# Optimization experiments

Hardware: AMD Instinct MI355X
Metric: run time of the kernel (lower is better)

The kernel has to match this reference:

```python
import jax, jax.numpy as jnp
import numpy as np

B, C, L = 4, 64, 4096

def setup_inputs() -> dict:
    key = jax.random.key(0)
    ks = jax.random.split(key, 7)
    s = 1.0 / np.sqrt(C)
    return {
        "x": jax.random.normal(ks[0], (B, C, L), dtype=jnp.float32),
        "wq": jax.random.uniform(ks[1], (C, C), jnp.float32, -s, s),
        "bq": jax.random.uniform(ks[2], (C,), jnp.float32, -s, s),
        "wk": jax.random.uniform(ks[3], (C, C), jnp.float32, -s, s),
        "bk": jax.random.uniform(ks[4], (C,), jnp.float32, -s, s),
        "wv": jax.random.uniform(ks[5], (C, C), jnp.float32, -s, s),
        "bv": jax.random.uniform(ks[6], (C,), jnp.float32, -s, s),
    }

def reference(x, wq, bq, wk, bk, wv, bv):
    # x: [B, C, L]; conv1d kernel-size-1 == per-position linear over channels.
    scale = jnp.sqrt(jnp.asarray(x.shape[1], x.dtype))
    # project and move to [B, L, C]
    q = jnp.einsum('oc,bcl->blo', wq, x) + bq  # [B, L, C]
    k = jnp.einsum('oc,bcl->blo', wk, x) + bk
    v = jnp.einsum('oc,bcl->blo', wv, x) + bv
    attn = jnp.einsum('bic,bjc->bij', q, k) / scale  # [B, L, L]
    attn = jax.nn.softmax(attn, axis=-1)
    out = jnp.einsum('bij,bjc->bic', attn, v)  # [B, L, C]
    return out.transpose(0, 2, 1) + x  # back to [B, C, L] with residual
```

## Files before the change

### kernel.cpp

```cpp
#include <hip/hip_runtime.h>
#include <hip/hip_bf16.h>

typedef float    f32x4  __attribute__((ext_vector_type(4)));
typedef float    f32x16 __attribute__((ext_vector_type(16)));
typedef short    s16x4  __attribute__((ext_vector_type(4)));
typedef short    s16x8  __attribute__((ext_vector_type(8)));
typedef unsigned u32x4  __attribute__((ext_vector_type(4)));
typedef __bf16   bf16x8 __attribute__((ext_vector_type(8)));

#define DEVI __device__ __forceinline__

DEVI short f2bf(float f) {
    unsigned u = __builtin_bit_cast(unsigned, f);
    u += 0x8000u;
    return (short)(u >> 16);
}
DEVI float bf2f(short s) {
    return __builtin_bit_cast(float, ((unsigned)(unsigned short)s) << 16);
}
DEVI unsigned cvt_pk_bf16(float lo, float hi) {
#if defined(__HIP_DEVICE_COMPILE__)
    unsigned r;
    asm("v_cvt_pk_bf16_f32 %0, %1, %2" : "=v"(r) : "v"(lo), "v"(hi));
    return r;
#else
    return (unsigned)(unsigned short)f2bf(lo) | ((unsigned)(unsigned short)f2bf(hi) << 16);
#endif
}

DEVI float fast_exp2(float x) {
#if defined(__HIP_DEVICE_COMPILE__) && __has_builtin(__builtin_amdgcn_exp2f)
    return __builtin_amdgcn_exp2f(x);
#else
    return exp2f(x);
#endif
}

DEVI f32x4 mfma32(s16x8 a, s16x8 b, f32x4 c) {
#if defined(__HIP_DEVICE_COMPILE__) && __has_builtin(__builtin_amdgcn_mfma_f32_16x16x32_bf16)
    return __builtin_amdgcn_mfma_f32_16x16x32_bf16(
        __builtin_bit_cast(bf16x8, a), __builtin_bit_cast(bf16x8, b), c, 0, 0, 0);
#else
    asm volatile("v_mfma_f32_16x16x32_bf16 %0, %1, %2, %0" : "+v"(c) : "v"(a), "v"(b));
    return c;
#endif
}

DEVI f32x16 mfma3216(s16x8 a, s16x8 b, f32x16 c) {
#if defined(__HIP_DEVICE_COMPILE__) && __has_builtin(__builtin_amdgcn_mfma_f32_32x32x16_bf16)
    return __builtin_amdgcn_mfma_f32_32x32x16_bf16(
        __builtin_bit_cast(bf16x8, a), __builtin_bit_cast(bf16x8, b), c, 0, 0, 0);
#else
    asm volatile("v_mfma_f32_32x32x16_bf16 %0, %1, %2, %0" : "+v"(c) : "v"(a), "v"(b));
    return c;
#endif
}

DEVI void setprio1() {
#if defined(__HIP_DEVICE_COMPILE__)
    __builtin_amdgcn_s_setprio(1);
#endif
}
DEVI void setprio0() {
#if defined(__HIP_DEVICE_COMPILE__)
    __builtin_amdgcn_s_setprio(0);
#endif
}

__global__ __launch_bounds__(512) void qkv_proj(
    const float* __restrict__ x,
    const float* __restrict__ wq, const float* __restrict__ bq,
    const float* __restrict__ wk, const float* __restrict__ bk,
    const float* __restrict__ wv, const float* __restrict__ bv,
    short* __restrict__ Qg, short* __restrict__ Kg, short* __restrict__ Vtg)
{
    __shared__ short Xt[32 * 64];

    const int b  = blockIdx.x >> 7;
    const int l0 = (blockIdx.x & 127) * 32;
    const int t  = threadIdx.x;
    const float QS = 0.18033688011112042f;

    {
        const int c  = t & 63;
        const int lh = (t >> 6) * 4;
        const float* xr = x + ((size_t)b * 64 + c) * 4096 + l0 + lh;
        const float4 x0 = *reinterpret_cast<const float4*>(xr);
        float xv[4] = {x0.x, x0.y, x0.z, x0.w};
        #pragma unroll
        for (int i = 0; i < 4; ++i) {
            const int l = lh + i;
            Xt[l * 64 + (((c >> 3) ^ (l & 7)) * 8) + (c & 7)] = f2bf(xv[i]);
        }
    }

    const int lane = t & 63, w = t >> 6;
    const int g = lane >> 4, col = lane & 15;
    const int o0 = (w & 3) * 16;
    const int h  = w >> 2;

    s16x8 wqf[2], wkf[2], wvf[2];
    #pragma unroll
    for (int kc = 0; kc < 2; ++kc) {
        const int cb = 8 * g + 32 * kc;
        const float4 q0 = *reinterpret_cast<const float4*>(wq + (o0 + col) * 64 + cb);
        const float4 q1 = *reinterpret_cast<const float4*>(wq + (o0 + col) * 64 + cb + 4);
        const float4 k0 = *reinterpret_cast<const float4*>(wk + (o0 + col) * 64 + cb);
        const float4 k1 = *reinterpret_cast<const float4*>(wk + (o0 + col) * 64 + cb + 4);
        const float4 v0 = *reinterpret_cast<const float4*>(wv + (o0 + col) * 64 + cb);
        const float4 v1 = *reinterpret_cast<const float4*>(wv + (o0 + col) * 64 + cb + 4);
        wqf[kc][0] = f2bf(q0.x * QS); wqf[kc][1] = f2bf(q0.y * QS);
        wqf[kc][2] = f2bf(q0.z * QS); wqf[kc][3] = f2bf(q0.w * QS);
        wqf[kc][4] = f2bf(q1.x * QS); wqf[kc][5] = f2bf(q1.y * QS);
        wqf[kc][6] = f2bf(q1.z * QS); wqf[kc][7] = f2bf(q1.w * QS);
        wkf[kc][0] = f2bf(k0.x); wkf[kc][1] = f2bf(k0.y);
        wkf[kc][2] = f2bf(k0.z); wkf[kc][3] = f2bf(k0.w);
        wkf[kc][4] = f2bf(k1.x); wkf[kc][5] = f2bf(k1.y);
        wkf[kc][6] = f2bf(k1.z); wkf[kc][7] = f2bf(k1.w);
        wvf[kc][0] = f2bf(v0.x); wvf[kc][1] = f2bf(v0.y);
        wvf[kc][2] = f2bf(v0.z); wvf[kc][3] = f2bf(v0.w);
        wvf[kc][4] = f2bf(v1.x); wvf[kc][5] = f2bf(v1.y);
        wvf[kc][6] = f2bf(v1.z); wvf[kc][7] = f2bf(v1.w);
    }
    const f32x4 bq4 = *reinterpret_cast<const f32x4*>(bq + o0 + 4 * g);
    const f32x4 bk4 = *reinterpret_cast<const f32x4*>(bk + o0 + 4 * g);
    const float bvs = bv[o0 + col];

    __syncthreads();

    {
        const int row = h * 16 + col;
        const s16x8 xf0 = *reinterpret_cast<const s16x8*>(
            &Xt[row * 64 + ((g ^ (row & 7)) * 8)]);
        const s16x8 xf1 = *reinterpret_cast<const s16x8*>(
            &Xt[row * 64 + (((g + 4) ^ (row & 7)) * 8)]);

        f32x4 qa = bq4 * QS;
        qa = mfma32(wqf[0], xf0, qa);
        qa = mfma32(wqf[1], xf1, qa);
        f32x4 ka = bk4;
        ka = mfma32(wkf[0], xf0, ka);
        ka = mfma32(wkf[1], xf1, ka);
        f32x4 va = {bvs, bvs, bvs, bvs};
        va = mfma32(xf0, wvf[0], va);
        va = mfma32(xf1, wvf[1], va);

        s16x4 qs, ks;
        #pragma unroll
        for (int r = 0; r < 4; ++r) { qs[r] = f2bf(qa[r]); ks[r] = f2bf(ka[r]); }
        const size_t qkbase = ((size_t)b * 4096 + l0 + row) * 64 + o0 + 4 * g;
        *reinterpret_cast<s16x4*>(Qg + qkbase) = qs;
        *reinterpret_cast<s16x4*>(Kg + qkbase) = ks;

        s16x4 vs;
        #pragma unroll
        for (int r = 0; r < 4; ++r) vs[r] = f2bf(va[r]);
        *reinterpret_cast<s16x4*>(
            Vtg + ((size_t)b * 64 + o0 + col) * 4096 + l0 + h * 16 + 4 * g) = vs;
    }
}

__global__ __launch_bounds__(512, 2) void attn_fused(
    const short* __restrict__ Qg, const short* __restrict__ Kg,
    const short* __restrict__ Vtg, const float* __restrict__ x,
    float* __restrict__ out)
{
    __shared__ short SM[73728];

    const int bid = blockIdx.x;
    const int wid = (bid & 7) * 32 + (bid >> 3);
    const int b   = wid >> 6;
    const int qt  = wid & 63;

    const int t    = threadIdx.x;
    const int w    = t >> 6;
    const int lane = t & 63;
    const int qi   = lane & 31;
    const int hi   = lane >> 5;
    const int rx   = qi & 7;
    const int kw   = w & 3;
    const int qw   = w >> 2;

    const int qglob = qt * 64 + qw * 32 + qi;

    s16x8 qf[4];
    {
        const short* qp = Qg + ((size_t)b * 4096 + qglob) * 64 + 8 * hi;
        qf[0] = *reinterpret_cast<const s16x8*>(qp);
        qf[1] = *reinterpret_cast<const s16x8*>(qp + 16);
        qf[2] = *reinterpret_cast<const s16x8*>(qp + 32);
        qf[3] = *reinterpret_cast<const s16x8*>(qp + 48);
    }

    const short* Kb = Kg  + (size_t)b * 4096 * 64;
    const short* Vb = Vtg + (size_t)b * 64 * 4096;

    const int r0k = lane >> 3;
    const int sk  = lane & 7;
    const int r0v = lane >> 2;
    const int sv  = lane & 3;

    short* Kbuf = SM + w * 9216;
    short* Vbuf = SM + w * 9216 + 4096;

    int kdoff[4], vdoff0[4], vdoff1[4];
    {
        const int dest0 = ((sv & 2) << 1) | (sv & 1);
        const int dest1 = dest0 | 2;
        #pragma unroll
        for (int c = 0; c < 4; ++c) {
            kdoff[c]  = (c * 8 + r0k) * 64 + ((sk ^ (r0k & 7)) * 8);
            vdoff0[c] = (c * 16 + r0v) * 40 + dest0 * 4;
            vdoff1[c] = (c * 16 + r0v) * 40 + dest1 * 4;
        }
    }
    const short* kgb = Kb + ((size_t)kw * 1024 + r0k) * 64 + sk * 8;
    const short* vgb = Vb + (size_t)r0v * 4096 + kw * 1024 + sv * 8;

    s16x8 kpre[4], vpre[4];
    #pragma unroll
    for (int c = 0; c < 4; ++c) {
        kpre[c] = *reinterpret_cast<const s16x8*>(kgb + c * 512);
        vpre[c] = *reinterpret_cast<const s16x8*>(vgb + (size_t)c * 65536);
    }
    #pragma unroll
    for (int c = 0; c < 4; ++c) {
        *reinterpret_cast<s16x8*>(&Kbuf[kdoff[c]]) = kpre[c];
        s16x4 vlo = {vpre[c][0], vpre[c][1], vpre[c][2], vpre[c][3]};
        s16x4 vhi = {vpre[c][4], vpre[c][5], vpre[c][6], vpre[c][7]};
        *reinterpret_cast<s16x4*>(&Vbuf[vdoff0[c]]) = vlo;
        *reinterpret_cast<s16x4*>(&Vbuf[vdoff1[c]]) = vhi;
    }

    f32x16 oacc0 = {}, oacc1 = {};
    float lsum = 0.0f;

    #pragma unroll 2
    for (int tt = 0; tt < 32; ++tt) {
        const int cur = tt & 1;
        const short* Kl = Kbuf + cur * 2048;
        const short* Vl = Vbuf + cur * 2560;

        if (tt < 31) {
            #pragma unroll
            for (int c = 0; c < 4; ++c) {
                kpre[c] = *reinterpret_cast<const s16x8*>(
                    kgb + (tt + 1) * 2048 + c * 512);
                vpre[c] = *reinterpret_cast<const s16x8*>(
                    vgb + (tt + 1) * 32 + (size_t)c * 65536);
            }
        }

        const short* kr = Kl + qi * 64;
        f32x16 S = {};
        setprio1();
        #pragma unroll
        for (int m = 0; m < 4; ++m) {
            const s16x8 a = *reinterpret_cast<const s16x8*>(
                kr + (((2 * m + hi) ^ rx) * 8));
            S = mfma3216(a, qf[m], S);
        }
        setprio0();

        const short* vr0 = Vl + qi * 40;
        const short* vr1 = Vl + (32 + qi) * 40;
        const s16x8 va00 = *reinterpret_cast<const s16x8*>(vr0 + hi * 8);
        const s16x8 va10 = *reinterpret_cast<const s16x8*>(vr1 + hi * 8);
        const s16x8 va01 = *reinterpret_cast<const s16x8*>(vr0 + (2 + hi) * 8);
        const s16x8 va11 = *reinterpret_cast<const s16x8*>(vr1 + (2 + hi) * 8);

        unsigned Pu[8];
        float ps = 0.0f;
        #pragma unroll
        for (int i = 0; i < 8; ++i) {
            const float e0 = fast_exp2(S[2 * i]);
            const float e1 = fast_exp2(S[2 * i + 1]);
            ps += e0 + e1;
            Pu[i] = cvt_pk_bf16(e0, e1);
        }
        lsum += ps;
        const u32x4 w0 = {Pu[0], Pu[1], Pu[2], Pu[3]};
        const u32x4 w1 = {Pu[4], Pu[5], Pu[6], Pu[7]};

        setprio1();
        oacc0 = mfma3216(va00, __builtin_bit_cast(s16x8, w0), oacc0);
        oacc1 = mfma3216(va10, __builtin_bit_cast(s16x8, w0), oacc1);
        oacc0 = mfma3216(va01, __builtin_bit_cast(s16x8, w1), oacc0);
        oacc1 = mfma3216(va11, __builtin_bit_cast(s16x8, w1), oacc1);
        setprio0();

        if (tt < 31) {
            short* Kd = Kbuf + (cur ^ 1) * 2048;
            short* Vd = Vbuf + (cur ^ 1) * 2560;
            #pragma unroll
            for (int c = 0; c < 4; ++c) {
                *reinterpret_cast<s16x8*>(&Kd[kdoff[c]]) = kpre[c];
                s16x4 vlo = {vpre[c][0], vpre[c][1], vpre[c][2], vpre[c][3]};
                s16x4 vhi = {vpre[c][4], vpre[c][5], vpre[c][6], vpre[c][7]};
                *reinterpret_cast<s16x4*>(&Vd[vdoff0[c]]) = vlo;
                *reinterpret_cast<s16x4*>(&Vd[vdoff1[c]]) = vhi;
            }
        }
    }

    const float ltot = lsum + __shfl_xor(lsum, 32);

    __syncthreads();
    float* Of = reinterpret_cast<float*>(SM);
    float* Lf = Of + 256 * 65;
    {
        const int rowb = (kw * 64 + qw * 32 + qi) * 65;
        #pragma unroll
        for (int db = 0; db < 2; ++db) {
            const f32x16 oa = db ? oacc1 : oacc0;
            #pragma unroll
            for (int r = 0; r < 16; ++r) {
                const int d = (r & 3) + 8 * (r >> 2) + 4 * hi + 32 * db;
                Of[rowb + d] = oa[r];
            }
        }
        if (hi == 0) Lf[kw * 64 + qw * 32 + qi] = ltot;
    }
    __syncthreads();

    {
        const int d  = t >> 3;
        const int q8 = (t & 7) * 8;
        float res[8];
        #pragma unroll
        for (int i = 0; i < 8; ++i) {
            const int rb = q8 + i;
            const float L = Lf[rb] + Lf[64 + rb] + Lf[128 + rb] + Lf[192 + rb];
            const float o = Of[(rb)       * 65 + d] + Of[(64 + rb)  * 65 + d] +
                            Of[(128 + rb) * 65 + d] + Of[(192 + rb) * 65 + d];
            res[i] = o / L;
        }
        const size_t ob = ((size_t)b * 64 + d) * 4096 + qt * 64 + q8;
        const float4 x0 = *reinterpret_cast<const float4*>(x + ob);
        const float4 x1 = *reinterpret_cast<const float4*>(x + ob + 4);
        float4 o0 = {res[0] + x0.x, res[1] + x0.y, res[2] + x0.z, res[3] + x0.w};
        float4 o1 = {res[4] + x1.x, res[5] + x1.y, res[6] + x1.z, res[7] + x1.w};
        *reinterpret_cast<float4*>(out + ob)     = o0;
        *reinterpret_cast<float4*>(out + ob + 4) = o1;
    }
}

extern "C" void kernel_launch(void* const* d_in, const int* in_sizes, int n_in,
                              void* d_out, int out_size, void* d_ws, size_t ws_size,
                              hipStream_t stream) {
    const float* x  = (const float*)d_in[0];
    const float* wq = (const float*)d_in[1];
    const float* bq = (const float*)d_in[2];
    const float* wk = (const float*)d_in[3];
    const float* bk = (const float*)d_in[4];
    const float* wv = (const float*)d_in[5];
    const float* bv = (const float*)d_in[6];
    float* out = (float*)d_out;

    short* Qg  = reinterpret_cast<short*>(d_ws);
    short* Kg  = Qg  + (size_t)4 * 4096 * 64;
    short* Vtg = Kg  + (size_t)4 * 4096 * 64;

    qkv_proj<<<dim3(512), dim3(512), 0, stream>>>(x, wq, bq, wk, bk, wv, bv, Qg, Kg, Vtg);
    attn_fused<<<dim3(256), dim3(512), 0, stream>>>(Qg, Kg, Vtg, x, out);
}
```

Measured before the change: 48.29 us.

## Split attention keys across 8 waves with shared cooperative K/V staging

The attention kernel grows from 512 to 1024 threads, so each block has 8 key-split waves per query half instead of 4, and each wave handles 16 tiles instead of 32. K/V tiles are now loaded cooperatively by 128-thread groups into shared buffers with padded rows (68/36 strides) instead of XOR swizzle. That needs a block-wide __syncthreads every tile. The final reduction now sums 8 partial outputs per query. This trades more parallelism and latency hiding per CU for extra block barriers, split 4-short LDS reads, and a larger cross-wave reduction.

```diff
diff --git a/kernel.cpp b/kernel.cpp
--- a/kernel.cpp
+++ b/kernel.cpp
@@ -14,9 +14,6 @@
     unsigned u = __builtin_bit_cast(unsigned, f);
     u += 0x8000u;
     return (short)(u >> 16);
-}
-DEVI float bf2f(short s) {
-    return __builtin_bit_cast(float, ((unsigned)(unsigned short)s) << 16);
 }
 DEVI unsigned cvt_pk_bf16(float lo, float hi) {
 #if defined(__HIP_DEVICE_COMPILE__)
@@ -160,12 +157,12 @@
     }
 }
 
-__global__ __launch_bounds__(512, 2) void attn_fused(
+__global__ __launch_bounds__(1024, 4) void attn_fused(
     const short* __restrict__ Qg, const short* __restrict__ Kg,
     const short* __restrict__ Vtg, const float* __restrict__ x,
     float* __restrict__ out)
 {
-    __shared__ short SM[73728];
+    __shared__ short SM[71680];
 
     const int bid = blockIdx.x;
     const int wid = (bid & 7) * 32 + (bid >> 3);
@@ -177,9 +174,8 @@
     const int lane = t & 63;
     const int qi   = lane & 31;
     const int hi   = lane >> 5;
-    const int rx   = qi & 7;
-    const int kw   = w & 3;
-    const int qw   = w >> 2;
+    const int kw   = w & 7;
+    const int qw   = w >> 3;
 
     const int qglob = qt * 64 + qw * 32 + qi;
 
@@ -195,79 +191,93 @@
     const short* Kb = Kg  + (size_t)b * 4096 * 64;
     const short* Vb = Vtg + (size_t)b * 64 * 4096;
 
-    const int r0k = lane >> 3;
-    const int sk  = lane & 7;
-    const int r0v = lane >> 2;
-    const int sv  = lane & 3;
-
-    short* Kbuf = SM + w * 9216;
-    short* Vbuf = SM + w * 9216 + 4096;
-
-    int kdoff[4], vdoff0[4], vdoff1[4];
-    {
-        const int dest0 = ((sv & 2) << 1) | (sv & 1);
-        const int dest1 = dest0 | 2;
-        #pragma unroll
-        for (int c = 0; c < 4; ++c) {
-            kdoff[c]  = (c * 8 + r0k) * 64 + ((sk ^ (r0k & 7)) * 8);
-            vdoff0[c] = (c * 16 + r0v) * 40 + dest0 * 4;
-            vdoff1[c] = (c * 16 + r0v) * 40 + dest1 * 4;
-        }
-    }
-    const short* kgb = Kb + ((size_t)kw * 1024 + r0k) * 64 + sk * 8;
-    const short* vgb = Vb + (size_t)r0v * 4096 + kw * 1024 + sv * 8;
-
-    s16x8 kpre[4], vpre[4];
-    #pragma unroll
-    for (int c = 0; c < 4; ++c) {
-        kpre[c] = *reinterpret_cast<const s16x8*>(kgb + c * 512);
-        vpre[c] = *reinterpret_cast<const s16x8*>(vgb + (size_t)c * 65536);
-    }
-    #pragma unroll
-    for (int c = 0; c < 4; ++c) {
-        *reinterpret_cast<s16x8*>(&Kbuf[kdoff[c]]) = kpre[c];
-        s16x4 vlo = {vpre[c][0], vpre[c][1], vpre[c][2], vpre[c][3]};
-        s16x4 vhi = {vpre[c][4], vpre[c][5], vpre[c][6], vpre[c][7]};
-        *reinterpret_cast<s16x4*>(&Vbuf[vdoff0[c]]) = vlo;
-        *reinterpret_cast<s16x4*>(&Vbuf[vdoff1[c]]) = vhi;
-    }
+    const int ks  = t >> 7;
+    const int tl  = t & 127;
+    const int kr0 = tl >> 3, ksl = tl & 7;
+    const int vr0 = tl >> 2, vch = tl & 3;
+    const int pgA = (vch & 2) * 2 + (vch & 1);
+    const int pgB = pgA + 2;
+
+    const short* kgb = Kb + ((size_t)ks * 512 + kr0) * 64 + ksl * 8;
+    const short* vgb = Vb + (size_t)vr0 * 4096 + ks * 512 + vch * 8;
+
+    const int kd0 = kr0 * 68 + ksl * 8;
+    const int kd1 = (kr0 + 16) * 68 + ksl * 8;
+    const int vd0 = vr0 * 36;
+    const int vd1 = (vr0 + 32) * 36;
+
+    s16x8 kpre0, kpre1, vpre0, vpre1;
+    kpre0 = *reinterpret_cast<const s16x8*>(kgb);
+    kpre1 = *reinterpret_cast<const s16x8*>(kgb + 1024);
+    vpre0 = *reinterpret_cast<const s16x8*>(vgb);
+    vpre1 = *reinterpret_cast<const s16x8*>(vgb + (size_t)32 * 4096);
+
+    {
+        short* Kd = SM + (ks * 2 + 0) * 2176;
+        short* Vd = SM + 34816 + (ks * 2 + 0) * 2304;
+        s16x4 a0 = {kpre0[0], kpre0[1], kpre0[2], kpre0[3]};
+        s16x4 a1 = {kpre0[4], kpre0[5], kpre0[6], kpre0[7]};
+        s16x4 a2 = {kpre1[0], kpre1[1], kpre1[2], kpre1[3]};
+        s16x4 a3 = {kpre1[4], kpre1[5], kpre1[6], kpre1[7]};
+        *reinterpret_cast<s16x4*>(Kd + kd0)     = a0;
+        *reinterpret_cast<s16x4*>(Kd + kd0 + 4) = a1;
+        *reinterpret_cast<s16x4*>(Kd + kd1)     = a2;
+        *reinterpret_cast<s16x4*>(Kd + kd1 + 4) = a3;
+        s16x4 b0 = {vpre0[0], vpre0[1], vpre0[2], vpre0[3]};
+        s16x4 b1 = {vpre0[4], vpre0[5], vpre0[6], vpre0[7]};
+        s16x4 b2 = {vpre1[0], vpre1[1], vpre1[2], vpre1[3]};
+        s16x4 b3 = {vpre1[4], vpre1[5], vpre1[6], vpre1[7]};
+        *reinterpret_cast<s16x4*>(Vd + vd0 + pgA * 4) = b0;
+        *reinterpret_cast<s16x4*>(Vd + vd0 + pgB * 4) = b1;
+        *reinterpret_cast<s16x4*>(Vd + vd1 + pgA * 4) = b2;
+        *reinterpret_cast<s16x4*>(Vd + vd1 + pgB * 4) = b3;
+    }
+    __syncthreads();
 
     f32x16 oacc0 = {}, oacc1 = {};
     float lsum = 0.0f;
 
     #pragma unroll 2
-    for (int tt = 0; tt < 32; ++tt) {
+    for (int tt = 0; tt < 16; ++tt) {
         const int cur = tt & 1;
-        const short* Kl = Kbuf + cur * 2048;
-        const short* Vl = Vbuf + cur * 2560;
-
-        if (tt < 31) {
-            #pragma unroll
-            for (int c = 0; c < 4; ++c) {
-                kpre[c] = *reinterpret_cast<const s16x8*>(
-                    kgb + (tt + 1) * 2048 + c * 512);
-                vpre[c] = *reinterpret_cast<const s16x8*>(
-                    vgb + (tt + 1) * 32 + (size_t)c * 65536);
-            }
-        }
-
-        const short* kr = Kl + qi * 64;
+        const short* Kl = SM + (kw * 2 + cur) * 2176;
+        const short* Vl = SM + 34816 + (kw * 2 + cur) * 2304;
+
+        if (tt < 15) {
+            kpre0 = *reinterpret_cast<const s16x8*>(kgb + (tt + 1) * 2048);
+            kpre1 = *reinterpret_cast<const s16x8*>(kgb + (tt + 1) * 2048 + 1024);
+            vpre0 = *reinterpret_cast<const s16x8*>(vgb + (tt + 1) * 32);
+            vpre1 = *reinterpret_cast<const s16x8*>(
+                vgb + (tt + 1) * 32 + (size_t)32 * 4096);
+        }
+
+        const short* kr = Kl + qi * 68;
         f32x16 S = {};
         setprio1();
         #pragma unroll
         for (int m = 0; m < 4; ++m) {
-            const s16x8 a = *reinterpret_cast<const s16x8*>(
-                kr + (((2 * m + hi) ^ rx) * 8));
+            const int off = (2 * m + hi) * 8;
+            const s16x4 alo = *reinterpret_cast<const s16x4*>(kr + off);
+            const s16x4 ahi = *reinterpret_cast<const s16x4*>(kr + off + 4);
+            const s16x8 a = {alo[0], alo[1], alo[2], alo[3],
+                             ahi[0], ahi[1], ahi[2], ahi[3]};
             S = mfma3216(a, qf[m], S);
         }
         setprio0();
 
-        const short* vr0 = Vl + qi * 40;
-        const short* vr1 = Vl + (32 + qi) * 40;
-        const s16x8 va00 = *reinterpret_cast<const s16x8*>(vr0 + hi * 8);
-        const s16x8 va10 = *reinterpret_cast<const s16x8*>(vr1 + hi * 8);
-        const s16x8 va01 = *reinterpret_cast<const s16x8*>(vr0 + (2 + hi) * 8);
-        const s16x8 va11 = *reinterpret_cast<const s16x8*>(vr1 + (2 + hi) * 8);
+        const short* vrA = Vl + qi * 36;
+        const short* vrB = Vl + (32 + qi) * 36;
+        s16x8 va[2][2];
+        #pragma unroll
+        for (int s = 0; s < 2; ++s) {
+            const int off = (2 * s + hi) * 8;
+            const s16x4 l0 = *reinterpret_cast<const s16x4*>(vrA + off);
+            const s16x4 h0 = *reinterpret_cast<const s16x4*>(vrA + off + 4);
+            const s16x4 l1 = *reinterpret_cast<const s16x4*>(vrB + off);
+            const s16x4 h1 = *reinterpret_cast<const s16x4*>(vrB + off + 4);
+            va[0][s] = s16x8{l0[0], l0[1], l0[2], l0[3], h0[0], h0[1], h0[2], h0[3]};
+            va[1][s] = s16x8{l1[0], l1[1], l1[2], l1[3], h1[0], h1[1], h1[2], h1[3]};
+        }
 
         unsigned Pu[8];
         float ps = 0.0f;
@@ -283,65 +293,74 @@
         const u32x4 w1 = {Pu[4], Pu[5], Pu[6], Pu[7]};
 
         setprio1();
-        oacc0 = mfma3216(va00, __builtin_bit_cast(s16x8, w0), oacc0);
-        oacc1 = mfma3216(va10, __builtin_bit_cast(s16x8, w0), oacc1);
-        oacc0 = mfma3216(va01, __builtin_bit_cast(s16x8, w1), oacc0);
-        oacc1 = mfma3216(va11, __builtin_bit_cast(s16x8, w1), oacc1);
+        oacc0 = mfma3216(va[0][0], __builtin_bit_cast(s16x8, w0), oacc0);
+        oacc1 = mfma3216(va[1][0], __builtin_bit_cast(s16x8, w0), oacc1);
+        oacc0 = mfma3216(va[0][1], __builtin_bit_cast(s16x8, w1), oacc0);
+        oacc1 = mfma3216(va[1][1], __builtin_bit_cast(s16x8, w1), oacc1);
         setprio0();
 
-        if (tt < 31) {
-            short* Kd = Kbuf + (cur ^ 1) * 2048;
-            short* Vd = Vbuf + (cur ^ 1) * 2560;
-            #pragma unroll
-            for (int c = 0; c < 4; ++c) {
-                *reinterpret_cast<s16x8*>(&Kd[kdoff[c]]) = kpre[c];
-                s16x4 vlo = {vpre[c][0], vpre[c][1], vpre[c][2], vpre[c][3]};
-                s16x4 vhi = {vpre[c][4], vpre[c][5], vpre[c][6], vpre[c][7]};
-                *reinterpret_cast<s16x4*>(&Vd[vdoff0[c]]) = vlo;
-                *reinterpret_cast<s16x4*>(&Vd[vdoff1[c]]) = vhi;
-            }
-        }
+        if (tt < 15) {
+            short* Kd = SM + (ks * 2 + (cur ^ 1)) * 2176;
+            short* Vd = SM + 34816 + (ks * 2 + (cur ^ 1)) * 2304;
+            s16x4 a0 = {kpre0[0], kpre0[1], kpre0[2], kpre0[3]};
+            s16x4 a1 = {kpre0[4], kpre0[5], kpre0[6], kpre0[7]};
+            s16x4 a2 = {kpre1[0], kpre1[1], kpre1[2], kpre1[3]};
+            s16x4 a3 = {kpre1[4], kpre1[5], kpre1[6], kpre1[7]};
+            *reinterpret_cast<s16x4*>(Kd + kd0)     = a0;
+            *reinterpret_cast<s16x4*>(Kd + kd0 + 4) = a1;
+            *reinterpret_cast<s16x4*>(Kd + kd1)     = a2;
+            *reinterpret_cast<s16x4*>(Kd + kd1 + 4) = a3;
+            s16x4 b0 = {vpre0[0], vpre0[1], vpre0[2], vpre0[3]};
+            s16x4 b1 = {vpre0[4], vpre0[5], vpre0[6], vpre0[7]};
+            s16x4 b2 = {vpre1[0], vpre1[1], vpre1[2], vpre1[3]};
+            s16x4 b3 = {vpre1[4], vpre1[5], vpre1[6], vpre1[7]};
+            *reinterpret_cast<s16x4*>(Vd + vd0 + pgA * 4) = b0;
+            *reinterpret_cast<s16x4*>(Vd + vd0 + pgB * 4) = b1;
+            *reinterpret_cast<s16x4*>(Vd + vd1 + pgA * 4) = b2;
+            *reinterpret_cast<s16x4*>(Vd + vd1 + pgB * 4) = b3;
+        }
+        __syncthreads();
     }
 
     const float ltot = lsum + __shfl_xor(lsum, 32);
 
     __syncthreads();
     float* Of = reinterpret_cast<float*>(SM);
-    float* Lf = Of + 256 * 65;
-    {
-        const int rowb = (kw * 64 + qw * 32 + qi) * 65;
+    float* Lf = Of + 512 * 66;
+    {
+        const int row = kw * 64 + qw * 32 + qi;
         #pragma unroll
         for (int db = 0; db < 2; ++db) {
             const f32x16 oa = db ? oacc1 : oacc0;
             #pragma unroll
             for (int r = 0; r < 16; ++r) {
                 const int d = (r & 3) + 8 * (r >> 2) + 4 * hi + 32 * db;
-                Of[rowb + d] = oa[r];
+                Of[row * 66 + d] = oa[r];
             }
         }
-        if (hi == 0) Lf[kw * 64 + qw * 32 + qi] = ltot;
+        if (hi == 0) Lf[row] = ltot;
     }
     __syncthreads();
 
     {
-        const int d  = t >> 3;
-        const int q8 = (t & 7) * 8;
-        float res[8];
-        #pragma unroll
-        for (int i = 0; i < 8; ++i) {
-            const int rb = q8 + i;
-            const float L = Lf[rb] + Lf[64 + rb] + Lf[128 + rb] + Lf[192 + rb];
-            const float o = Of[(rb)       * 65 + d] + Of[(64 + rb)  * 65 + d] +
-                            Of[(128 + rb) * 65 + d] + Of[(192 + rb) * 65 + d];
-            res[i] = o / L;
-        }
-        const size_t ob = ((size_t)b * 64 + d) * 4096 + qt * 64 + q8;
-        const float4 x0 = *reinterpret_cast<const float4*>(x + ob);
-        const float4 x1 = *reinterpret_cast<const float4*>(x + ob + 4);
-        float4 o0 = {res[0] + x0.x, res[1] + x0.y, res[2] + x0.z, res[3] + x0.w};
-        float4 o1 = {res[4] + x1.x, res[5] + x1.y, res[6] + x1.z, res[7] + x1.w};
-        *reinterpret_cast<float4*>(out + ob)     = o0;
-        *reinterpret_cast<float4*>(out + ob + 4) = o1;
+        const int d  = t >> 4;
+        const int qc = (t & 15) * 4;
+        float res[4];
+        #pragma unroll
+        for (int j = 0; j < 4; ++j) {
+            const int q = qc + j;
+            float L = 0.0f, o = 0.0f;
+            #pragma unroll
+            for (int s = 0; s < 8; ++s) {
+                L += Lf[s * 64 + q];
+                o += Of[(s * 64 + q) * 66 + d];
+            }
+            res[j] = o / L;
+        }
+        const size_t ob = ((size_t)b * 64 + d) * 4096 + qt * 64 + qc;
+        const float4 xv = *reinterpret_cast<const float4*>(x + ob);
+        float4 o4 = {res[0] + xv.x, res[1] + xv.y, res[2] + xv.z, res[3] + xv.w};
+        *reinterpret_cast<float4*>(out + ob) = o4;
     }
 }
 
@@ -362,5 +381,5 @@
     short* Vtg = Kg  + (size_t)4 * 4096 * 64;
 
     qkv_proj<<<dim3(512), dim3(512), 0, stream>>>(x, wq, bq, wk, bk, wv, bv, Qg, Kg, Vtg);
-    attn_fused<<<dim3(256), dim3(512), 0, stream>>>(Qg, Kg, Vtg, x, out);
-}
+    attn_fused<<<dim3(256), dim3(1024), 0, stream>>>(Qg, Kg, Vtg, x, out);
+}
```

New measurement: 56.62 us. 1.17x slower.

## Share K/V tiles across query waves to shrink LDS and double occupancy

Applied to the files above, without the earlier changes.

The attention kernel previously gave each wave private double-buffered K/V tiles in shared memory (about 144KB per block). Now the K/V stages are shared by the two query-waves that cover the same key split, loaded cooperatively and guarded by a block barrier each iteration. This cuts LDS to 64KB and raises the launch-bounds occupancy target from 2 to 4 blocks. The V layout changes from a padded to an XOR-swizzled layout, and the final cross-wave reduction stages partial outputs in bf16 with a reciprocal normalize. In exchange it adds a __syncthreads per iteration, tighter register limits, and some precision loss in the partial sums.

```diff
diff --git a/kernel.cpp b/kernel.cpp
--- a/kernel.cpp
+++ b/kernel.cpp
@@ -5,6 +5,7 @@
 typedef float    f32x16 __attribute__((ext_vector_type(16)));
 typedef short    s16x4  __attribute__((ext_vector_type(4)));
 typedef short    s16x8  __attribute__((ext_vector_type(8)));
+typedef unsigned u32x2  __attribute__((ext_vector_type(2)));
 typedef unsigned u32x4  __attribute__((ext_vector_type(4)));
 typedef __bf16   bf16x8 __attribute__((ext_vector_type(8)));
 
@@ -160,12 +161,12 @@
     }
 }
 
-__global__ __launch_bounds__(512, 2) void attn_fused(
+__global__ __launch_bounds__(512, 4) void attn_fused(
     const short* __restrict__ Qg, const short* __restrict__ Kg,
     const short* __restrict__ Vtg, const float* __restrict__ x,
     float* __restrict__ out)
 {
-    __shared__ short SM[73728];
+    __shared__ short SM[32768];
 
     const int bid = blockIdx.x;
     const int wid = (bid & 7) * 32 + (bid >> 3);
@@ -177,7 +178,6 @@
     const int lane = t & 63;
     const int qi   = lane & 31;
     const int hi   = lane >> 5;
-    const int rx   = qi & 7;
     const int kw   = w & 3;
     const int qw   = w >> 2;
 
@@ -195,60 +195,68 @@
     const short* Kb = Kg  + (size_t)b * 4096 * 64;
     const short* Vb = Vtg + (size_t)b * 64 * 4096;
 
-    const int r0k = lane >> 3;
-    const int sk  = lane & 7;
-    const int r0v = lane >> 2;
-    const int sv  = lane & 3;
-
-    short* Kbuf = SM + w * 9216;
-    short* Vbuf = SM + w * 9216 + 4096;
-
-    int kdoff[4], vdoff0[4], vdoff1[4];
-    {
-        const int dest0 = ((sv & 2) << 1) | (sv & 1);
-        const int dest1 = dest0 | 2;
-        #pragma unroll
-        for (int c = 0; c < 4; ++c) {
-            kdoff[c]  = (c * 8 + r0k) * 64 + ((sk ^ (r0k & 7)) * 8);
-            vdoff0[c] = (c * 16 + r0v) * 40 + dest0 * 4;
-            vdoff1[c] = (c * 16 + r0v) * 40 + dest1 * 4;
-        }
-    }
-    const short* kgb = Kb + ((size_t)kw * 1024 + r0k) * 64 + sk * 8;
-    const short* vgb = Vb + (size_t)r0v * 4096 + kw * 1024 + sv * 8;
-
-    s16x8 kpre[4], vpre[4];
-    #pragma unroll
-    for (int c = 0; c < 4; ++c) {
-        kpre[c] = *reinterpret_cast<const s16x8*>(kgb + c * 512);
-        vpre[c] = *reinterpret_cast<const s16x8*>(vgb + (size_t)c * 65536);
-    }
-    #pragma unroll
-    for (int c = 0; c < 4; ++c) {
-        *reinterpret_cast<s16x8*>(&Kbuf[kdoff[c]]) = kpre[c];
-        s16x4 vlo = {vpre[c][0], vpre[c][1], vpre[c][2], vpre[c][3]};
-        s16x4 vhi = {vpre[c][4], vpre[c][5], vpre[c][6], vpre[c][7]};
-        *reinterpret_cast<s16x4*>(&Vbuf[vdoff0[c]]) = vlo;
-        *reinterpret_cast<s16x4*>(&Vbuf[vdoff1[c]]) = vhi;
-    }
+    const int ks  = t >> 7;
+    const int tl  = t & 127;
+    const int kr0 = tl >> 3, ksl = tl & 7;
+    const int vd  = tl >> 2, vs = tl & 3;
+
+    const int kswz = (ksl ^ (kr0 & 7)) * 8;
+    const int kd0  = kr0 * 64 + kswz;
+    const int kd1  = (kr0 + 16) * 64 + kswz;
+    const int vkey = (vd >> 1) & 3;
+    const int g0G  = (((vs >> 1) * 2) ^ vkey);
+    const int g1G  = (((vs >> 1) * 2 + 1) ^ vkey);
+    const int vp   = (vs & 1) * 4;
+    const int vdo0 = vd * 32 + g0G * 8 + vp;
+    const int vdo1 = vd * 32 + g1G * 8 + vp;
+    const int vdo2 = (vd + 32) * 32 + g0G * 8 + vp;
+    const int vdo3 = (vd + 32) * 32 + g1G * 8 + vp;
+
+    const short* kgb = Kb + ((size_t)ks * 1024 + kr0) * 64 + ksl * 8;
+    const short* vgb = Vb + (size_t)vd * 4096 + ks * 1024 + vs * 8;
+
+    short* Kst = SM + ks * 2 * 2048;
+    short* Vst = SM + 16384 + ks * 2 * 2048;
+
+    s16x8 kpre0, kpre1, vpre0, vpre1;
+    kpre0 = *reinterpret_cast<const s16x8*>(kgb);
+    kpre1 = *reinterpret_cast<const s16x8*>(kgb + 16 * 64);
+    vpre0 = *reinterpret_cast<const s16x8*>(vgb);
+    vpre1 = *reinterpret_cast<const s16x8*>(vgb + (size_t)32 * 4096);
+    {
+        *reinterpret_cast<s16x8*>(&Kst[kd0]) = kpre0;
+        *reinterpret_cast<s16x8*>(&Kst[kd1]) = kpre1;
+        s16x4 a0 = {vpre0[0], vpre0[1], vpre0[2], vpre0[3]};
+        s16x4 a1 = {vpre0[4], vpre0[5], vpre0[6], vpre0[7]};
+        s16x4 a2 = {vpre1[0], vpre1[1], vpre1[2], vpre1[3]};
+        s16x4 a3 = {vpre1[4], vpre1[5], vpre1[6], vpre1[7]};
+        *reinterpret_cast<s16x4*>(&Vst[vdo0]) = a0;
+        *reinterpret_cast<s16x4*>(&Vst[vdo1]) = a1;
+        *reinterpret_cast<s16x4*>(&Vst[vdo2]) = a2;
+        *reinterpret_cast<s16x4*>(&Vst[vdo3]) = a3;
+    }
+    __syncthreads();
 
     f32x16 oacc0 = {}, oacc1 = {};
     float lsum = 0.0f;
+
+    const short* Kc = SM + kw * 2 * 2048;
+    const short* Vc = SM + 16384 + kw * 2 * 2048;
+    const int rx  = qi & 7;
+    const int vky = (qi >> 1) & 3;
 
     #pragma unroll 2
     for (int tt = 0; tt < 32; ++tt) {
         const int cur = tt & 1;
-        const short* Kl = Kbuf + cur * 2048;
-        const short* Vl = Vbuf + cur * 2560;
+        const short* Kl = Kc + cur * 2048;
+        const short* Vl = Vc + cur * 2048;
 
         if (tt < 31) {
-            #pragma unroll
-            for (int c = 0; c < 4; ++c) {
-                kpre[c] = *reinterpret_cast<const s16x8*>(
-                    kgb + (tt + 1) * 2048 + c * 512);
-                vpre[c] = *reinterpret_cast<const s16x8*>(
-                    vgb + (tt + 1) * 32 + (size_t)c * 65536);
-            }
+            kpre0 = *reinterpret_cast<const s16x8*>(kgb + (tt + 1) * 2048);
+            kpre1 = *reinterpret_cast<const s16x8*>(kgb + (tt + 1) * 2048 + 1024);
+            vpre0 = *reinterpret_cast<const s16x8*>(vgb + (tt + 1) * 32);
+            vpre1 = *reinterpret_cast<const s16x8*>(
+                vgb + (tt + 1) * 32 + (size_t)32 * 4096);
         }
 
         const short* kr = Kl + qi * 64;
@@ -262,12 +270,14 @@
         }
         setprio0();
 
-        const short* vr0 = Vl + qi * 40;
-        const short* vr1 = Vl + (32 + qi) * 40;
-        const s16x8 va00 = *reinterpret_cast<const s16x8*>(vr0 + hi * 8);
-        const s16x8 va10 = *reinterpret_cast<const s16x8*>(vr1 + hi * 8);
-        const s16x8 va01 = *reinterpret_cast<const s16x8*>(vr0 + (2 + hi) * 8);
-        const s16x8 va11 = *reinterpret_cast<const s16x8*>(vr1 + (2 + hi) * 8);
+        const short* vrA = Vl + qi * 32;
+        const short* vrB = Vl + (32 + qi) * 32;
+        const int gs0 = ((0 + hi) ^ vky) * 8;
+        const int gs1 = ((2 + hi) ^ vky) * 8;
+        const s16x8 vaA0 = *reinterpret_cast<const s16x8*>(vrA + gs0);
+        const s16x8 vaB0 = *reinterpret_cast<const s16x8*>(vrB + gs0);
+        const s16x8 vaA1 = *reinterpret_cast<const s16x8*>(vrA + gs1);
+        const s16x8 vaB1 = *reinterpret_cast<const s16x8*>(vrB + gs1);
 
         unsigned Pu[8];
         float ps = 0.0f;
@@ -283,40 +293,45 @@
         const u32x4 w1 = {Pu[4], Pu[5], Pu[6], Pu[7]};
 
         setprio1();
-        oacc0 = mfma3216(va00, __builtin_bit_cast(s16x8, w0), oacc0);
-        oacc1 = mfma3216(va10, __builtin_bit_cast(s16x8, w0), oacc1);
-        oacc0 = mfma3216(va01, __builtin_bit_cast(s16x8, w1), oacc0);
-        oacc1 = mfma3216(va11, __builtin_bit_cast(s16x8, w1), oacc1);
+        oacc0 = mfma3216(vaA0, __builtin_bit_cast(s16x8, w0), oacc0);
+        oacc1 = mfma3216(vaB0, __builtin_bit_cast(s16x8, w0), oacc1);
+        oacc0 = mfma3216(vaA1, __builtin_bit_cast(s16x8, w1), oacc0);
+        oacc1 = mfma3216(vaB1, __builtin_bit_cast(s16x8, w1), oacc1);
         setprio0();
 
         if (tt < 31) {
-            short* Kd = Kbuf + (cur ^ 1) * 2048;
-            short* Vd = Vbuf + (cur ^ 1) * 2560;
-            #pragma unroll
-            for (int c = 0; c < 4; ++c) {
-                *reinterpret_cast<s16x8*>(&Kd[kdoff[c]]) = kpre[c];
-                s16x4 vlo = {vpre[c][0], vpre[c][1], vpre[c][2], vpre[c][3]};
-                s16x4 vhi = {vpre[c][4], vpre[c][5], vpre[c][6], vpre[c][7]};
-                *reinterpret_cast<s16x4*>(&Vd[vdoff0[c]]) = vlo;
-                *reinterpret_cast<s16x4*>(&Vd[vdoff1[c]]) = vhi;
-            }
-        }
+            short* Kd = Kst + (cur ^ 1) * 2048;
+            short* Vd = Vst + (cur ^ 1) * 2048;
+            *reinterpret_cast<s16x8*>(&Kd[kd0]) = kpre0;
+            *reinterpret_cast<s16x8*>(&Kd[kd1]) = kpre1;
+            s16x4 a0 = {vpre0[0], vpre0[1], vpre0[2], vpre0[3]};
+            s16x4 a1 = {vpre0[4], vpre0[5], vpre0[6], vpre0[7]};
+            s16x4 a2 = {vpre1[0], vpre1[1], vpre1[2], vpre1[3]};
+            s16x4 a3 = {vpre1[4], vpre1[5], vpre1[6], vpre1[7]};
+            *reinterpret_cast<s16x4*>(&Vd[vdo0]) = a0;
+            *reinterpret_cast<s16x4*>(&Vd[vdo1]) = a1;
+            *reinterpret_cast<s16x4*>(&Vd[vdo2]) = a2;
+            *reinterpret_cast<s16x4*>(&Vd[vdo3]) = a3;
+        }
+        __syncthreads();
     }
 
     const float ltot = lsum + __shfl_xor(lsum, 32);
 
-    __syncthreads();
-    float* Of = reinterpret_cast<float*>(SM);
-    float* Lf = Of + 256 * 65;
-    {
-        const int rowb = (kw * 64 + qw * 32 + qi) * 65;
+    short* Po = SM;
+    float* Lf = reinterpret_cast<float*>(SM + 256 * 68);
+    {
+        const int row = kw * 64 + qw * 32 + qi;
         #pragma unroll
         for (int db = 0; db < 2; ++db) {
             const f32x16 oa = db ? oacc1 : oacc0;
             #pragma unroll
-            for (int r = 0; r < 16; ++r) {
-                const int d = (r & 3) + 8 * (r >> 2) + 4 * hi + 32 * db;
-                Of[rowb + d] = oa[r];
+            for (int rq = 0; rq < 4; ++rq) {
+                u32x2 pk;
+                pk[0] = cvt_pk_bf16(oa[4 * rq + 0], oa[4 * rq + 1]);
+                pk[1] = cvt_pk_bf16(oa[4 * rq + 2], oa[4 * rq + 3]);
+                const int dbase = 8 * rq + 4 * hi + 32 * db;
+                *reinterpret_cast<u32x2*>(&Po[row * 68 + dbase]) = pk;
             }
         }
         if (hi == 0) Lf[kw * 64 + qw * 32 + qi] = ltot;
@@ -324,24 +339,29 @@
     __syncthreads();
 
     {
-        const int d  = t >> 3;
-        const int q8 = (t & 7) * 8;
-        float res[8];
+        const int q  = t & 63;
+        const int ds = (t >> 6) * 8;
+        float acc[8] = {};
+        float L = 0.0f;
+        #pragma unroll
+        for (int s = 0; s < 4; ++s) {
+            const int row = s * 64 + q;
+            L += Lf[row];
+            const s16x4 o0 = *reinterpret_cast<const s16x4*>(&Po[row * 68 + ds]);
+            const s16x4 o1 = *reinterpret_cast<const s16x4*>(&Po[row * 68 + ds + 4]);
+            #pragma unroll
+            for (int i = 0; i < 4; ++i) {
+                acc[i]     += bf2f(o0[i]);
+                acc[4 + i] += bf2f(o1[i]);
+            }
+        }
+        const float rL = 1.0f / L;
+        const size_t ob = ((size_t)b * 64 + ds) * 4096 + qt * 64 + q;
         #pragma unroll
         for (int i = 0; i < 8; ++i) {
-            const int rb = q8 + i;
-            const float L = Lf[rb] + Lf[64 + rb] + Lf[128 + rb] + Lf[192 + rb];
-            const float o = Of[(rb)       * 65 + d] + Of[(64 + rb)  * 65 + d] +
-                            Of[(128 + rb) * 65 + d] + Of[(192 + rb) * 65 + d];
-            res[i] = o / L;
-        }
-        const size_t ob = ((size_t)b * 64 + d) * 4096 + qt * 64 + q8;
-        const float4 x0 = *reinterpret_cast<const float4*>(x + ob);
-        const float4 x1 = *reinterpret_cast<const float4*>(x + ob + 4);
-        float4 o0 = {res[0] + x0.x, res[1] + x0.y, res[2] + x0.z, res[3] + x0.w};
-        float4 o1 = {res[4] + x1.x, res[5] + x1.y, res[6] + x1.z, res[7] + x1.w};
-        *reinterpret_cast<float4*>(out + ob)     = o0;
-        *reinterpret_cast<float4*>(out + ob + 4) = o1;
+            const size_t idx = ob + (size_t)i * 4096;
+            out[idx] = fmaf(acc[i], rL, x[idx]);
+        }
     }
 }
 
```

Measured after the change: 71.79 us. 1.49x slower.
